# Kernel optimization log

Hardware: AMD Instinct MI355X
Metric: run time of the kernel (lower is better)

The kernel has to match this reference:

```python
import jax, jax.numpy as jnp
import numpy as np

N = 50000   # nodes
E = 800000  # edges
D = 128     # hidden_dim
LN_EPS = 1e-5


def _mlp2(x, W1, b1, W2, b2, act_last):
    y = jax.nn.silu(x @ W1 + b1)
    y = y @ W2 + b2
    return jax.nn.silu(y) if act_last else y


def setup_inputs() -> dict:
    key = jax.random.key(0)
    ks = jax.random.split(key, 20)
    s = 1.0 / np.sqrt(D)
    inp = {
        "h": jax.random.normal(ks[0], (N, D), jnp.float32),
        "x": jax.random.normal(ks[1], (N, 3), jnp.float32),
        "vel_all": jax.random.normal(ks[2], (N, 5, 3), jnp.float32),
        "edge_index": jax.random.randint(ks[3], (2, E), 0, N, jnp.int64),
        # phi_e: Linear(2D+11, D) -> SiLU -> Linear(D, D) -> SiLU   (weights stored [in,out])
        "We1": jax.random.uniform(ks[4], (2 * D + 11, D), jnp.float32, -s, s),
        "be1": jax.random.uniform(ks[5], (D,), jnp.float32, -s, s),
        "We2": jax.random.uniform(ks[6], (D, D), jnp.float32, -s, s),
        "be2": jax.random.uniform(ks[7], (D,), jnp.float32, -s, s),
        # phi_x: Linear(D, D) -> SiLU -> Linear(D, 1)
        "Wx1": jax.random.uniform(ks[8], (D, D), jnp.float32, -s, s),
        "bx1": jax.random.uniform(ks[9], (D,), jnp.float32, -s, s),
        "Wx2": jax.random.uniform(ks[10], (D, 1), jnp.float32, -s, s),
        "bx2": jax.random.uniform(ks[11], (1,), jnp.float32, -s, s),
        # phi_h: Linear(2D, D) -> SiLU -> Linear(D, D)
        "Wh1": jax.random.uniform(ks[12], (2 * D, D), jnp.float32, -s, s),
        "bh1": jax.random.uniform(ks[13], (D,), jnp.float32, -s, s),
        "Wh2": jax.random.uniform(ks[14], (D, D), jnp.float32, -s, s),
        "bh2": jax.random.uniform(ks[15], (D,), jnp.float32, -s, s),
        # LayerNorm(D)
        "gamma": jnp.ones((D,), jnp.float32),
        "beta": jnp.zeros((D,), jnp.float32),
    }
    return inp


def reference(h, x, vel_all, edge_index, We1, be1, We2, be2, Wx1, bx1, Wx2, bx2,
              Wh1, bh1, Wh2, bh2, gamma, beta):
    n = h.shape[0]
    src, dst = edge_index[0], edge_index[1]

    rel = x[src] - x[dst]                                  # [E,3]
    dist2 = jnp.sum(rel * rel, axis=-1, keepdims=True)     # [E,1]
    dist = jnp.maximum(jnp.sqrt(dist2), 1e-8)
    r_hat = rel / dist                                     # [E,3]

    vel_proj_src = jnp.sum(vel_all[src] * r_hat[:, None, :], axis=-1)  # [E,5]
    vel_proj_dst = jnp.sum(vel_all[dst] * r_hat[:, None, :], axis=-1)  # [E,5]

    feat = jnp.concatenate([h[src], h[dst], dist2, vel_proj_src, vel_proj_dst], axis=-1)
    m_ij = _mlp2(feat, We1, be1, We2, be2, act_last=True)  # [E,D]

    # update_coords=True: scatter_mean of rel * phi_x(m_ij)
    coord_w = _mlp2(m_ij, Wx1, bx1, Wx2, bx2, act_last=False)          # [E,1]
    num = jax.ops.segment_sum(rel * coord_w, dst, num_segments=n)      # [N,3]
    cnt = jax.ops.segment_sum(jnp.ones((rel.shape[0], 1), x.dtype), dst, num_segments=n)
    delta_x = num / jnp.maximum(cnt, 1.0)
    x = x + delta_x

    agg = jax.ops.segment_sum(m_ij, dst, num_segments=n)               # [N,D]
    dh = _mlp2(jnp.concatenate([h, agg], axis=-1), Wh1, bh1, Wh2, bh2, act_last=False)
    h = h + dh  # dropout=0 -> identity

    # LayerNorm
    mu = jnp.mean(h, axis=-1, keepdims=True)
    var = jnp.mean(jnp.square(h - mu), axis=-1, keepdims=True)
    h = (h - mu) * jax.lax.rsqrt(var + LN_EPS) * gamma + beta

    return (h, x, m_ij)
```

## Files before the change

### kernel.cpp

```cpp
#include <hip/hip_runtime.h>
#include <stdint.h>

#define CAPB 64

typedef __attribute__((ext_vector_type(8))) short bf16x8;
typedef __attribute__((ext_vector_type(4))) float f32x4;

__device__ __forceinline__ float bf2f(unsigned short u){
  union { unsigned int i; float f; } v; v.i = ((unsigned int)u) << 16; return v.f;
}
__device__ __forceinline__ unsigned short f2bf(float f){
  union { float f; unsigned int i; } v; v.f = f;
  unsigned int x = v.i;
  unsigned int r = (x + 0x7FFFu + ((x >> 16) & 1u)) >> 16;
  return (unsigned short)r;
}
__device__ __forceinline__ float silu_f(float v){
  return v / (1.0f + __expf(-v));
}

template<bool F32> __device__ __forceinline__ float ldv(const void* p, size_t i){
  if (F32) return ((const float*)p)[i];
  return bf2f(((const unsigned short*)p)[i]);
}
template<bool F32> __device__ __forceinline__ void stv(void* p, size_t i, float v){
  if (F32) ((float*)p)[i] = v;
  else     ((unsigned short*)p)[i] = f2bf(v);
}
template<bool I64> __device__ __forceinline__ int ldidx(const int* p, size_t i){
  return I64 ? p[2*i] : p[i];
}

__global__ void detect_kernel(const unsigned int* gw, const int* eidx, int N, int* flags){
  int f = 0;
  if (gw[0] == 0x3F800000u) f |= 1;
  bool i64 = true;
  for (int k = 0; k < 4; k++){
    int lo = eidx[2*k], hi = eidx[2*k+1];
    if (hi != 0 || lo < 0 || lo >= N) i64 = false;
  }
  if (i64) f |= 2;
  flags[0] = f;
}

__global__ __launch_bounds__(256) void hist_kernel(
    const int* eidx, int* cnt_i, int* bucket, int* slot, int N, int E, const int* flags)
{
  int e = blockIdx.x * 256 + threadIdx.x;
  if (e >= E) return;
  int d;
  if (flags[0] & 2) d = eidx[2*((size_t)E + e)];
  else              d = eidx[(size_t)E + e];
  d = min(max(d, 0), N-1);
  int p = atomicAdd(&cnt_i[d], 1);
  slot[e] = p;
  if (p < CAPB) bucket[(size_t)d*CAPB + p] = e;
}

struct __align__(16) NodePreSmem { float hlt[128][36]; };

template<bool F32>
__device__ void node_pre_impl(NodePreSmem& S, const void* h, const void* We1,
                              unsigned short* H1a, unsigned short* H1b, int N)
{
  const int t = threadIdx.x;
  const int base = blockIdx.x * 32;
  for (int i = t; i < 32*128; i += 256){
    int nl = i >> 7, j = i & 127;
    int node = base + nl;
    S.hlt[j][nl] = (node < N) ? ldv<F32>(h, (size_t)node*128 + j) : 0.0f;
  }
  __syncthreads();
  const int j = t & 127, half = t >> 7;
  const size_t wbase = (size_t)(half * 128) * 128;
  unsigned short* O = half ? H1b : H1a;
  float acc[32];
  #pragma unroll
  for (int nl=0; nl<32; nl++) acc[nl] = 0.0f;
  #pragma unroll 2
  for (int k=0; k<128; k++){
    float w = ldv<F32>(We1, wbase + (size_t)k*128 + j);
    const float4* row = (const float4*)&S.hlt[k][0];
    #pragma unroll
    for (int g=0; g<8; g++){
      float4 hv = row[g];
      acc[g*4+0] += hv.x * w;
      acc[g*4+1] += hv.y * w;
      acc[g*4+2] += hv.z * w;
      acc[g*4+3] += hv.w * w;
    }
  }
  #pragma unroll
  for (int nl=0; nl<32; nl++){
    int node = base + nl;
    if (node < N) O[(size_t)node*128 + j] = f2bf(acc[nl]);
  }
}

__global__ __launch_bounds__(256) void node_pre(
    const void* h, const void* We1, unsigned short* H1a, unsigned short* H1b,
    int N, const int* flags)
{
  __shared__ NodePreSmem S;
  if (flags[0] & 1) node_pre_impl<true >(S, h, We1, H1a, H1b, N);
  else              node_pre_impl<false>(S, h, We1, H1a, H1b, N);
}

template<bool F32, bool I64, bool M1F32>
__device__ void m1_impl(
    const void* xu, const void* velu, const int* eidx,
    const unsigned short* __restrict__ H1a, const unsigned short* __restrict__ H1b,
    const void* We1, const void* be1,
    void* m1p, int N, int E)
{
  const int t = threadIdx.x;
  const int sub = t & 31;
  const int j0 = sub * 4;
  float gw[11][4];
  #pragma unroll
  for (int k=0;k<11;k++)
    #pragma unroll
    for (int c=0;c<4;c++) gw[k][c] = ldv<F32>(We1, (size_t)(256+k)*128 + j0 + c);
  float b1[4];
  #pragma unroll
  for (int c=0;c<4;c++) b1[c] = ldv<F32>(be1, j0 + c);

  int gid = blockIdx.x * 8 + (t >> 5);
  const int gstride = gridDim.x * 8;
  for (int e = gid; e < E; e += gstride){
    int s = ldidx<I64>(eidx, e);
    int d = ldidx<I64>(eidx, (size_t)E + e);
    s = min(max(s, 0), N-1);
    d = min(max(d, 0), N-1);
    float rx = ldv<F32>(xu,(size_t)s*3+0) - ldv<F32>(xu,(size_t)d*3+0);
    float ry = ldv<F32>(xu,(size_t)s*3+1) - ldv<F32>(xu,(size_t)d*3+1);
    float rz = ldv<F32>(xu,(size_t)s*3+2) - ldv<F32>(xu,(size_t)d*3+2);
    float dist2 = rx*rx + ry*ry + rz*rz;
    float dist = fmaxf(sqrtf(dist2), 1e-8f);
    float inv = 1.0f / dist;
    float ux = rx*inv, uy = ry*inv, uz = rz*inv;
    float geo[11];
    geo[0] = dist2;
    #pragma unroll
    for (int v=0; v<5; v++){
      geo[1+v] = ldv<F32>(velu,(size_t)s*15+v*3+0)*ux + ldv<F32>(velu,(size_t)s*15+v*3+1)*uy + ldv<F32>(velu,(size_t)s*15+v*3+2)*uz;
      geo[6+v] = ldv<F32>(velu,(size_t)d*15+v*3+0)*ux + ldv<F32>(velu,(size_t)d*15+v*3+1)*uy + ldv<F32>(velu,(size_t)d*15+v*3+2)*uz;
    }
    uint2 ua = *(const uint2*)&H1a[(size_t)s*128 + j0];
    uint2 ub = *(const uint2*)&H1b[(size_t)d*128 + j0];
    float a[4];
    a[0] = bf2f((unsigned short)(ua.x & 0xFFFFu)) + bf2f((unsigned short)(ub.x & 0xFFFFu)) + b1[0];
    a[1] = bf2f((unsigned short)(ua.x >> 16))     + bf2f((unsigned short)(ub.x >> 16))     + b1[1];
    a[2] = bf2f((unsigned short)(ua.y & 0xFFFFu)) + bf2f((unsigned short)(ub.y & 0xFFFFu)) + b1[2];
    a[3] = bf2f((unsigned short)(ua.y >> 16))     + bf2f((unsigned short)(ub.y >> 16))     + b1[3];
    #pragma unroll
    for (int k=0;k<11;k++){
      float g = geo[k];
      #pragma unroll
      for (int c=0;c<4;c++) a[c] += gw[k][c] * g;
    }
    #pragma unroll
    for (int c=0;c<4;c++) a[c] = silu_f(a[c]);
    if (M1F32){
      float4 v = { a[0], a[1], a[2], a[3] };
      *(float4*)((float*)m1p + (size_t)e*128 + j0) = v;
    } else {
      uint2 p;
      p.x = (unsigned int)f2bf(a[0]) | ((unsigned int)f2bf(a[1]) << 16);
      p.y = (unsigned int)f2bf(a[2]) | ((unsigned int)f2bf(a[3]) << 16);
      *(uint2*)((unsigned short*)m1p + (size_t)e*128 + j0) = p;
    }
  }
}

template<bool USE_WS>
__global__ __launch_bounds__(256) void m1_kernel(
    const void* xu, const void* velu, const int* eidx,
    const unsigned short* H1a, const unsigned short* H1b,
    const void* We1, const void* be1,
    void* m1ws, void* out, size_t moff, int N, int E, const int* flags)
{
  int f = flags[0];
  if (USE_WS){
    if      (f == 0) m1_impl<false,false,false>(xu,velu,eidx,H1a,H1b,We1,be1,m1ws,N,E);
    else if (f == 1) m1_impl<true ,false,false>(xu,velu,eidx,H1a,H1b,We1,be1,m1ws,N,E);
    else if (f == 2) m1_impl<false,true ,false>(xu,velu,eidx,H1a,H1b,We1,be1,m1ws,N,E);
    else             m1_impl<true ,true ,false>(xu,velu,eidx,H1a,H1b,We1,be1,m1ws,N,E);
  } else {
    if (f & 1){
      void* p = (void*)((float*)out + moff);
      if (f & 2) m1_impl<true,true ,true>(xu,velu,eidx,H1a,H1b,We1,be1,p,N,E);
      else       m1_impl<true,false,true>(xu,velu,eidx,H1a,H1b,We1,be1,p,N,E);
    } else {
      void* p = (void*)((unsigned short*)out + moff);
      if (f & 2) m1_impl<false,true ,false>(xu,velu,eidx,H1a,H1b,We1,be1,p,N,E);
      else       m1_impl<false,false,false>(xu,velu,eidx,H1a,H1b,We1,be1,p,N,E);
    }
  }
}

struct __align__(16) GemmSmem {
  unsigned short m1s[64][136];
  unsigned short m2s[64][136];
  float relv[192];
  int   dsts[64];
  int   slot[64];
  float wpart[4][64];
};

template<bool F32, bool I64, bool M1F32>
__device__ void gemm_impl(GemmSmem& S,
    const void* xu, const int* eidx, const void* m1p,
    const void* We2, const void* be2, const void* Wx1, const void* bx1,
    const void* Wx2, const void* bx2,
    void* out, size_t moff,
    float* __restrict__ agg, float* __restrict__ num,
    const int* __restrict__ slotp,
    int N, int E, int ntiles)
{
  const int t = threadIdx.x;
  const int wave = t >> 6, lane = t & 63;
  const int col = lane & 15, quad = lane >> 4;
  const int colbase = wave * 32;

  bf16x8 bwe2[2][4], bwx1[2][4];
  float wx2v[2], be2v[2], bx1v[2];
  #pragma unroll
  for (int nt=0; nt<2; nt++){
    int n = colbase + nt*16 + col;
    wx2v[nt] = ldv<F32>(Wx2, n);
    be2v[nt] = ldv<F32>(be2, n);
    bx1v[nt] = ldv<F32>(bx1, n);
    #pragma unroll
    for (int kb=0; kb<4; kb++){
      bf16x8 a, b;
      #pragma unroll
      for (int jj=0; jj<8; jj++){
        int k = kb*32 + quad*8 + jj;
        a[jj] = (short)f2bf(ldv<F32>(We2, (size_t)k*128 + n));
        b[jj] = (short)f2bf(ldv<F32>(Wx1, (size_t)k*128 + n));
      }
      bwe2[nt][kb] = a; bwx1[nt][kb] = b;
    }
  }
  const int jfix = t & 127;
  const float bx2v = ldv<F32>(bx2, 0);
  const int srow = t >> 2, sseg = t & 3;

  for (int tile = blockIdx.x; tile < ntiles; tile += gridDim.x){
    const int ebase = tile * 64;
    {
      const int e = ebase + srow;
      if (M1F32){
        const float* rp = (const float*)m1p + (size_t)e*128 + sseg*32;
        #pragma unroll
        for (int q=0;q<4;q++){
          float4 va = {0,0,0,0}, vb = {0,0,0,0};
          if (e < E){ va = *(const float4*)(rp + q*8); vb = *(const float4*)(rp + q*8 + 4); }
          bf16x8 w;
          w[0]=(short)f2bf(va.x); w[1]=(short)f2bf(va.y); w[2]=(short)f2bf(va.z); w[3]=(short)f2bf(va.w);
          w[4]=(short)f2bf(vb.x); w[5]=(short)f2bf(vb.y); w[6]=(short)f2bf(vb.z); w[7]=(short)f2bf(vb.w);
          *(bf16x8*)&S.m1s[srow][sseg*32 + q*8] = w;
        }
      } else {
        const unsigned short* rp = (const unsigned short*)m1p + (size_t)e*128 + sseg*32;
        #pragma unroll
        for (int q=0;q<4;q++){
          bf16x8 w = {0,0,0,0,0,0,0,0};
          if (e < E) w = *(const bf16x8*)(rp + q*8);
          *(bf16x8*)&S.m1s[srow][sseg*32 + q*8] = w;
        }
      }
      if (t < 64){
        int e2 = ebase + t;
        int s2 = 0, d2 = 0, sl = 0;
        if (e2 < E){
          s2 = ldidx<I64>(eidx, e2);
          d2 = ldidx<I64>(eidx, (size_t)E + e2);
          sl = slotp[e2];
        }
        s2 = min(max(s2,0), N-1); d2 = min(max(d2,0), N-1);
        S.dsts[t] = d2; S.slot[t] = sl;
        S.relv[t*3+0] = ldv<F32>(xu,(size_t)s2*3+0) - ldv<F32>(xu,(size_t)d2*3+0);
        S.relv[t*3+1] = ldv<F32>(xu,(size_t)s2*3+1) - ldv<F32>(xu,(size_t)d2*3+1);
        S.relv[t*3+2] = ldv<F32>(xu,(size_t)s2*3+2) - ldv<F32>(xu,(size_t)d2*3+2);
      }
    }
    __syncthreads();
    #pragma unroll
    for (int et=0; et<4; et++){
      #pragma unroll
      for (int nt=0; nt<2; nt++){
        f32x4 acc = { be2v[nt], be2v[nt], be2v[nt], be2v[nt] };
        #pragma unroll
        for (int kb=0; kb<4; kb++){
          bf16x8 a = *(const bf16x8*)&S.m1s[et*16 + col][kb*32 + quad*8];
          acc = __builtin_amdgcn_mfma_f32_16x16x32_bf16(a, bwe2[nt][kb], acc, 0, 0, 0);
        }
        int n = colbase + nt*16 + col;
        #pragma unroll
        for (int r=0; r<4; r++)
          S.m2s[et*16 + quad*4 + r][n] = f2bf(silu_f(acc[r]));
      }
    }
    __syncthreads();
    if (F32){
      #pragma unroll
      for (int it=0; it<4; it++){
        const int sl = t + it*256;
        const int el = sl >> 4, i8 = sl & 15;
        const int e = ebase + el;
        if (e < E){
          const bf16x8 mv = *(const bf16x8*)&S.m2s[el][i8*8];
          float f[8];
          #pragma unroll
          for (int j=0; j<8; j++) f[j] = bf2f((unsigned short)mv[j]);
          float* op = (float*)out + moff + (size_t)e*128 + i8*8;
          float4 v0 = { f[0], f[1], f[2], f[3] };
          float4 v1 = { f[4], f[5], f[6], f[7] };
          *(float4*)op = v0;
          *(float4*)(op + 4) = v1;
          if (S.slot[el] >= CAPB){
            float* ap = &agg[(size_t)S.dsts[el]*128 + i8*8];
            #pragma unroll
            for (int j=0; j<8; j++) atomicAdd(ap + j, f[j]);
          }
        }
      }
    } else {
      #pragma unroll
      for (int it=0; it<32; it++){
        int el = (t + it*256) >> 7;
        int e = ebase + el;
        if (e < E){
          float v = bf2f(S.m2s[el][jfix]);
          stv<F32>(out, moff + (size_t)e*128 + jfix, v);
          atomicAdd(&agg[(size_t)S.dsts[el]*128 + jfix], v);
        }
      }
    }
    float part[4][4];
    #pragma unroll
    for (int et=0; et<4; et++)
      #pragma unroll
      for (int r=0; r<4; r++) part[et][r] = 0.0f;
    #pragma unroll
    for (int et=0; et<4; et++){
      #pragma unroll
      for (int nt=0; nt<2; nt++){
        f32x4 acc = { bx1v[nt], bx1v[nt], bx1v[nt], bx1v[nt] };
        #pragma unroll
        for (int kb=0; kb<4; kb++){
          bf16x8 a = *(const bf16x8*)&S.m2s[et*16 + col][kb*32 + quad*8];
          acc = __builtin_amdgcn_mfma_f32_16x16x32_bf16(a, bwx1[nt][kb], acc, 0, 0, 0);
        }
        #pragma unroll
        for (int r=0; r<4; r++) part[et][r] += silu_f(acc[r]) * wx2v[nt];
      }
    }
    #pragma unroll
    for (int et=0; et<4; et++){
      #pragma unroll
      for (int r=0; r<4; r++){
        float v = part[et][r];
        v += __shfl_xor(v, 1, 16);
        v += __shfl_xor(v, 2, 16);
        v += __shfl_xor(v, 4, 16);
        v += __shfl_xor(v, 8, 16);
        part[et][r] = v;
      }
    }
    if (col == 0){
      #pragma unroll
      for (int et=0; et<4; et++)
        #pragma unroll
        for (int r=0; r<4; r++)
          S.wpart[wave][et*16 + quad*4 + r] = part[et][r];
    }
    __syncthreads();
    if (t < 64){
      int e = ebase + t;
      if (e < E){
        float w = S.wpart[0][t] + S.wpart[1][t] + S.wpart[2][t] + S.wpart[3][t] + bx2v;
        int d = S.dsts[t];
        atomicAdd(&num[(size_t)d*3+0], S.relv[t*3+0]*w);
        atomicAdd(&num[(size_t)d*3+1], S.relv[t*3+1]*w);
        atomicAdd(&num[(size_t)d*3+2], S.relv[t*3+2]*w);
      }
    }
    __syncthreads();
  }
}

template<bool USE_WS>
__global__ __launch_bounds__(256) void gemm_kernel(
    const void* xu, const int* eidx, const void* m1ws,
    const void* We2, const void* be2, const void* Wx1, const void* bx1,
    const void* Wx2, const void* bx2,
    void* out, size_t moff, float* agg, float* num, const int* slotp,
    int N, int E, int ntiles, const int* flags)
{
  __shared__ GemmSmem S;
  int f = flags[0];
  if (USE_WS){
    if      (f == 0) gemm_impl<false,false,false>(S, xu, eidx, m1ws, We2,be2,Wx1,bx1,Wx2,bx2, out,moff, agg,num, slotp, N,E,ntiles);
    else if (f == 1) gemm_impl<true ,false,false>(S, xu, eidx, m1ws, We2,be2,Wx1,bx1,Wx2,bx2, out,moff, agg,num, slotp, N,E,ntiles);
    else if (f == 2) gemm_impl<false,true ,false>(S, xu, eidx, m1ws, We2,be2,Wx1,bx1,Wx2,bx2, out,moff, agg,num, slotp, N,E,ntiles);
    else             gemm_impl<true ,true ,false>(S, xu, eidx, m1ws, We2,be2,Wx1,bx1,Wx2,bx2, out,moff, agg,num, slotp, N,E,ntiles);
  } else {
    if (f & 1){
      const void* p = (const void*)((float*)out + moff);
      if (f & 2) gemm_impl<true,true ,true>(S, xu, eidx, p, We2,be2,Wx1,bx1,Wx2,bx2, out,moff, agg,num, slotp, N,E,ntiles);
      else       gemm_impl<true,false,true>(S, xu, eidx, p, We2,be2,Wx1,bx1,Wx2,bx2, out,moff, agg,num, slotp, N,E,ntiles);
    } else {
      const void* p = (const void*)((unsigned short*)out + moff);
      if (f & 2) gemm_impl<false,true ,false>(S, xu, eidx, p, We2,be2,Wx1,bx1,Wx2,bx2, out,moff, agg,num, slotp, N,E,ntiles);
      else       gemm_impl<false,false,false>(S, xu, eidx, p, We2,be2,Wx1,bx1,Wx2,bx2, out,moff, agg,num, slotp, N,E,ntiles);
    }
  }
}

struct __align__(16) NodeFinalSmem {
  unsigned short ins[16][256];
  unsigned short y1s[16][128];
  float hns[16][128];
};

template<bool F32>
__device__ void node_final_impl(NodeFinalSmem& S,
    const void* h, const void* xu,
    const float* __restrict__ agg, const float* __restrict__ num,
    const int* __restrict__ cnt_i, const int* __restrict__ bucket,
    const void* Wh1, const void* bh1, const void* Wh2, const void* bh2,
    const void* gam, const void* bet,
    void* out, size_t xoff, size_t moff, int N)
{
  const int t = threadIdx.x;
  const int base = blockIdx.x * 16;
  for (int i = t; i < 16*128; i += 256){
    int n = i >> 7, c = i & 127;
    int node = base + n;
    S.ins[n][c] = (node < N) ? f2bf(ldv<F32>(h, (size_t)node*128 + c)) : (unsigned short)0;
  }
  if (F32){
    const int g = t >> 4, i8 = t & 15;
    const int lanebase = (t & 63) & ~15;
    const int node = base + g;
    float a[8] = {0,0,0,0,0,0,0,0};
    if (node < N){
      int deg = cnt_i[node];
      int kmax = min(deg, CAPB);
      const float* mbase = (const float*)out + moff;
      for (int c0 = 0; c0 < kmax; c0 += 16){
        int ee = 0;
        if (c0 + i8 < kmax) ee = bucket[(size_t)node*CAPB + c0 + i8];
        int cnum = min(16, kmax - c0);
        #pragma unroll
        for (int k = 0; k < 16; k++){
          if (k < cnum){
            int e = __shfl(ee, lanebase + k, 64);
            const float* rp = mbase + (size_t)e*128 + i8*8;
            float4 v0 = *(const float4*)rp;
            float4 v1 = *(const float4*)(rp + 4);
            a[0]+=v0.x; a[1]+=v0.y; a[2]+=v0.z; a[3]+=v0.w;
            a[4]+=v1.x; a[5]+=v1.y; a[6]+=v1.z; a[7]+=v1.w;
          }
        }
      }
      if (deg > CAPB){
        const float* ap = &agg[(size_t)node*128 + i8*8];
        #pragma unroll
        for (int j=0; j<8; j++) a[j] += ap[j];
      }
    }
    #pragma unroll
    for (int j=0; j<8; j++) S.ins[g][128 + i8*8 + j] = f2bf(a[j]);
  } else {
    for (int i = t; i < 16*128; i += 256){
      int n = i >> 7, c = i & 127;
      int node = base + n;
      S.ins[n][128 + c] = (node < N) ? f2bf(agg[(size_t)node*128 + c]) : (unsigned short)0;
    }
  }
  __syncthreads();
  const int j = t & 127, nh = t >> 7;
  {
    float acc[8];
    #pragma unroll
    for (int u=0; u<8; u++) acc[u] = ldv<F32>(bh1, j);
    #pragma unroll 4
    for (int k=0; k<256; k++){
      float w = ldv<F32>(Wh1, (size_t)k*128 + j);
      #pragma unroll
      for (int u=0; u<8; u++) acc[u] += bf2f(S.ins[nh + 2*u][k]) * w;
    }
    #pragma unroll
    for (int u=0; u<8; u++) S.y1s[nh + 2*u][j] = f2bf(silu_f(acc[u]));
  }
  __syncthreads();
  {
    float acc[8];
    #pragma unroll
    for (int u=0; u<8; u++) acc[u] = ldv<F32>(bh2, j);
    #pragma unroll 4
    for (int k=0; k<128; k++){
      float w = ldv<F32>(Wh2, (size_t)k*128 + j);
      #pragma unroll
      for (int u=0; u<8; u++) acc[u] += bf2f(S.y1s[nh + 2*u][k]) * w;
    }
    #pragma unroll
    for (int u=0; u<8; u++){
      int n = nh + 2*u;
      int node = base + n;
      float hv = (node < N) ? ldv<F32>(h, (size_t)node*128 + j) : 0.0f;
      S.hns[n][j] = hv + acc[u];
    }
  }
  __syncthreads();
  {
    int n = t >> 4, sub = t & 15;
    float s = 0.0f, ss = 0.0f;
    #pragma unroll
    for (int i2=0; i2<8; i2++){
      float v = S.hns[n][sub + 16*i2];
      s += v; ss += v*v;
    }
    #pragma unroll
    for (int m=1; m<16; m<<=1){ s += __shfl_xor(s, m, 16); ss += __shfl_xor(ss, m, 16); }
    float mu = s * (1.0f/128.0f);
    float var = fmaxf(ss * (1.0f/128.0f) - mu*mu, 0.0f);
    float rs = rsqrtf(var + 1e-5f);
    int gnode = base + n;
    if (gnode < N){
      #pragma unroll
      for (int i2=0; i2<8; i2++){
        int jj = sub + 16*i2;
        float v = (S.hns[n][jj] - mu) * rs * ldv<F32>(gam, jj) + ldv<F32>(bet, jj);
        stv<F32>(out, (size_t)gnode*128 + jj, v);
      }
    }
  }
  if (t < 48){
    int n = t / 3, c = t % 3;
    int node = base + n;
    if (node < N){
      float cv = fmaxf((float)cnt_i[node], 1.0f);
      float dx = num[(size_t)node*3 + c] / cv;
      stv<F32>(out, xoff + (size_t)node*3 + c, ldv<F32>(xu, (size_t)node*3 + c) + dx);
    }
  }
}

__global__ __launch_bounds__(256) void node_final(
    const void* h, const void* xu,
    const float* agg, const float* num, const int* cnt_i, const int* bucket,
    const void* Wh1, const void* bh1, const void* Wh2, const void* bh2,
    const void* gam, const void* bet,
    void* out, size_t xoff, size_t moff, int N, const int* flags)
{
  __shared__ NodeFinalSmem S;
  if (flags[0] & 1) node_final_impl<true >(S, h, xu, agg, num, cnt_i, bucket, Wh1, bh1, Wh2, bh2, gam, bet, out, xoff, moff, N);
  else              node_final_impl<false>(S, h, xu, agg, num, cnt_i, bucket, Wh1, bh1, Wh2, bh2, gam, bet, out, xoff, moff, N);
}

extern "C" void kernel_launch(void* const* d_in, const int* in_sizes, int n_in,
                              void* d_out, int out_size, void* d_ws, size_t ws_size,
                              hipStream_t stream)
{
  const int N = in_sizes[0] / 128;
  const int E = in_sizes[3] / 2;

  char* ws = (char*)d_ws;
  int* flags = (int*)ws;
  size_t off = 256;
  unsigned short* H1a = (unsigned short*)(ws + off); off += (size_t)N*256;
  unsigned short* H1b = (unsigned short*)(ws + off); off += (size_t)N*256;
  float* agg   = (float*)(ws + off); off += (size_t)N*512;
  float* num   = (float*)(ws + off); off += (size_t)N*12;
  int*   cnt_i = (int*)(ws + off); off += (size_t)N*4;
  int*   bucket= (int*)(ws + off); off += (size_t)N*CAPB*4;
  int*   slot  = (int*)(ws + off); off += (size_t)E*4;
  void*  m1ws  = (void*)(ws + off); off += (size_t)E*256;
  const bool use_ws = (off <= ws_size);

  detect_kernel<<<1, 1, 0, stream>>>((const unsigned int*)d_in[16], (const int*)d_in[3], N, flags);

  size_t zbytes = (size_t)N*512 + (size_t)N*12 + (size_t)N*4;
  hipMemsetAsync((void*)agg, 0, zbytes, stream);

  hist_kernel<<<(E + 255) / 256, 256, 0, stream>>>((const int*)d_in[3], cnt_i, bucket, slot, N, E, flags);

  node_pre<<<(N + 31) / 32, 256, 0, stream>>>(d_in[0], d_in[4], H1a, H1b, N, flags);

  size_t xoff = (size_t)N * 128;
  size_t moff = (size_t)N * 128 + (size_t)N * 3;
  int ntiles = (E + 63) / 64;

  if (use_ws){
    m1_kernel<true><<<2048, 256, 0, stream>>>(d_in[1], d_in[2], (const int*)d_in[3], H1a, H1b,
                                              d_in[4], d_in[5], m1ws, d_out, moff, N, E, flags);
    gemm_kernel<true><<<2500, 256, 0, stream>>>(d_in[1], (const int*)d_in[3], m1ws,
                                                d_in[6], d_in[7], d_in[8], d_in[9],
                                                d_in[10], d_in[11],
                                                d_out, moff, agg, num, slot, N, E, ntiles, flags);
  } else {
    m1_kernel<false><<<2048, 256, 0, stream>>>(d_in[1], d_in[2], (const int*)d_in[3], H1a, H1b,
                                               d_in[4], d_in[5], m1ws, d_out, moff, N, E, flags);
    gemm_kernel<false><<<2500, 256, 0, stream>>>(d_in[1], (const int*)d_in[3], m1ws,
                                                 d_in[6], d_in[7], d_in[8], d_in[9],
                                                 d_in[10], d_in[11],
                                                 d_out, moff, agg, num, slot, N, E, ntiles, flags);
  }

  node_final<<<(N + 15) / 16, 256, 0, stream>>>(d_in[0], d_in[1], agg, num, cnt_i, bucket,
                                                d_in[12], d_in[13], d_in[14], d_in[15],
                                                d_in[16], d_in[17],
                                                d_out, xoff, moff, N, flags);
}
```

Measured before the change: 1.311 ms.

## Software-pipeline m1 tile loads and defer coord atomics in edge GEMM kernel

Adds a specialized fp32-input path for the edge GEMM kernel. It prefetches the next tile's bf16 m1 rows and edge indices into registers while the current tile runs its MFMA work. The num coordinate atomics are deferred by one iteration so they overlap the next tile's setup instead of needing an extra barrier. This costs more registers per thread, which may lower occupancy, and makes the loop carry state across iterations.

```diff
diff --git a/kernel.cpp b/kernel.cpp
--- a/kernel.cpp
+++ b/kernel.cpp
@@ -207,6 +207,172 @@
   int   slot[64];
   float wpart[4][64];
 };
+
+template<bool I64>
+__device__ void gemm_async_impl(GemmSmem& S,
+    const float* __restrict__ xu, const int* __restrict__ eidx,
+    const unsigned short* __restrict__ m1p,
+    const float* __restrict__ We2, const float* __restrict__ be2,
+    const float* __restrict__ Wx1, const float* __restrict__ bx1,
+    const float* __restrict__ Wx2, const float* __restrict__ bx2,
+    float* __restrict__ out, size_t moff,
+    float* __restrict__ agg, float* __restrict__ num,
+    const int* __restrict__ slotp,
+    int N, int E, int ntiles)
+{
+  const int t = threadIdx.x;
+  const int wave = t >> 6, lane = t & 63;
+  const int col = lane & 15, quad = lane >> 4;
+  const int colbase = wave * 32;
+
+  bf16x8 bwe2[2][4], bwx1[2][4];
+  float wx2v[2], be2v[2], bx1v[2];
+  #pragma unroll
+  for (int nt=0; nt<2; nt++){
+    int n = colbase + nt*16 + col;
+    wx2v[nt] = Wx2[n]; be2v[nt] = be2[n]; bx1v[nt] = bx1[n];
+    #pragma unroll
+    for (int kb=0; kb<4; kb++){
+      bf16x8 a, b;
+      #pragma unroll
+      for (int jj=0; jj<8; jj++){
+        int k = kb*32 + quad*8 + jj;
+        a[jj] = (short)f2bf(We2[(size_t)k*128 + n]);
+        b[jj] = (short)f2bf(Wx1[(size_t)k*128 + n]);
+      }
+      bwe2[nt][kb] = a; bwx1[nt][kb] = b;
+    }
+  }
+  const float bx2v = bx2[0];
+  const int srow = t >> 2, sseg = t & 3;
+  const int gs = gridDim.x;
+
+  bf16x8 r0, r1, r2, r3;
+  int nsv = 0, ndv = 0, nsl = 0;
+  float prx = 0, pry = 0, prz = 0;
+  int pdst = 0, pvalid = 0, have_w = 0;
+
+  int tile = blockIdx.x;
+  if (tile < ntiles){
+    size_t e = (size_t)tile*64 + srow; if (e >= (size_t)E) e = (size_t)E - 1;
+    const unsigned short* rp = m1p + e*128 + (size_t)sseg*32;
+    r0 = *(const bf16x8*)(rp);      r1 = *(const bf16x8*)(rp + 8);
+    r2 = *(const bf16x8*)(rp + 16); r3 = *(const bf16x8*)(rp + 24);
+    if (t < 64){
+      int ec = min(tile*64 + t, E-1);
+      nsv = ldidx<I64>(eidx, ec);
+      ndv = ldidx<I64>(eidx, (size_t)E + ec);
+      nsl = slotp[ec];
+    }
+  }
+
+  for (; tile < ntiles; tile += gs){
+    const int ebase = tile * 64;
+    if (t < 64){
+      if (have_w && pvalid){
+        float w = S.wpart[0][t] + S.wpart[1][t] + S.wpart[2][t] + S.wpart[3][t] + bx2v;
+        atomicAdd(&num[(size_t)pdst*3+0], prx*w);
+        atomicAdd(&num[(size_t)pdst*3+1], pry*w);
+        atomicAdd(&num[(size_t)pdst*3+2], prz*w);
+      }
+      int s = min(max(nsv, 0), N-1), d = min(max(ndv, 0), N-1);
+      S.dsts[t] = d; S.slot[t] = nsl;
+      pvalid = (ebase + t) < E; pdst = d;
+      prx = xu[(size_t)s*3+0] - xu[(size_t)d*3+0];
+      pry = xu[(size_t)s*3+1] - xu[(size_t)d*3+1];
+      prz = xu[(size_t)s*3+2] - xu[(size_t)d*3+2];
+    }
+    *(bf16x8*)&S.m1s[srow][sseg*32 +  0] = r0;
+    *(bf16x8*)&S.m1s[srow][sseg*32 +  8] = r1;
+    *(bf16x8*)&S.m1s[srow][sseg*32 + 16] = r2;
+    *(bf16x8*)&S.m1s[srow][sseg*32 + 24] = r3;
+    if (tile + gs < ntiles){
+      size_t e = (size_t)(tile+gs)*64 + srow; if (e >= (size_t)E) e = (size_t)E - 1;
+      const unsigned short* rp = m1p + e*128 + (size_t)sseg*32;
+      r0 = *(const bf16x8*)(rp);      r1 = *(const bf16x8*)(rp + 8);
+      r2 = *(const bf16x8*)(rp + 16); r3 = *(const bf16x8*)(rp + 24);
+      if (t < 64){
+        int ec = min((tile+gs)*64 + t, E-1);
+        nsv = ldidx<I64>(eidx, ec);
+        ndv = ldidx<I64>(eidx, (size_t)E + ec);
+        nsl = slotp[ec];
+      }
+    }
+    __syncthreads();
+    const int erem = E - ebase;
+    #pragma unroll
+    for (int et=0; et<4; et++){
+      #pragma unroll
+      for (int nt=0; nt<2; nt++){
+        f32x4 acc = { be2v[nt], be2v[nt], be2v[nt], be2v[nt] };
+        #pragma unroll
+        for (int kb=0; kb<4; kb++){
+          bf16x8 a = *(const bf16x8*)&S.m1s[et*16 + col][kb*32 + quad*8];
+          acc = __builtin_amdgcn_mfma_f32_16x16x32_bf16(a, bwe2[nt][kb], acc, 0, 0, 0);
+        }
+        int n = colbase + nt*16 + col;
+        #pragma unroll
+        for (int r=0; r<4; r++){
+          int el = et*16 + quad*4 + r;
+          float v = silu_f(acc[r]);
+          S.m2s[el][n] = f2bf(v);
+          if (el < erem){
+            out[moff + (size_t)(ebase + el)*128 + n] = v;
+            if (S.slot[el] >= CAPB)
+              atomicAdd(&agg[(size_t)S.dsts[el]*128 + n], v);
+          }
+        }
+      }
+    }
+    __syncthreads();
+    float part[4][4];
+    #pragma unroll
+    for (int et=0; et<4; et++)
+      #pragma unroll
+      for (int r=0; r<4; r++) part[et][r] = 0.0f;
+    #pragma unroll
+    for (int et=0; et<4; et++){
+      #pragma unroll
+      for (int nt=0; nt<2; nt++){
+        f32x4 acc = { bx1v[nt], bx1v[nt], bx1v[nt], bx1v[nt] };
+        #pragma unroll
+        for (int kb=0; kb<4; kb++){
+          bf16x8 a = *(const bf16x8*)&S.m2s[et*16 + col][kb*32 + quad*8];
+          acc = __builtin_amdgcn_mfma_f32_16x16x32_bf16(a, bwx1[nt][kb], acc, 0, 0, 0);
+        }
+        #pragma unroll
+        for (int r=0; r<4; r++) part[et][r] += silu_f(acc[r]) * wx2v[nt];
+      }
+    }
+    #pragma unroll
+    for (int et=0; et<4; et++){
+      #pragma unroll
+      for (int r=0; r<4; r++){
+        float v = part[et][r];
+        v += __shfl_xor(v, 1, 16);
+        v += __shfl_xor(v, 2, 16);
+        v += __shfl_xor(v, 4, 16);
+        v += __shfl_xor(v, 8, 16);
+        part[et][r] = v;
+      }
+    }
+    if (col == 0){
+      #pragma unroll
+      for (int et=0; et<4; et++)
+        #pragma unroll
+        for (int r=0; r<4; r++)
+          S.wpart[wave][et*16 + quad*4 + r] = part[et][r];
+    }
+    __syncthreads();
+    have_w = 1;
+  }
+  if (t < 64 && have_w && pvalid){
+    float w = S.wpart[0][t] + S.wpart[1][t] + S.wpart[2][t] + S.wpart[3][t] + bx2v;
+    atomicAdd(&num[(size_t)pdst*3+0], prx*w);
+    atomicAdd(&num[(size_t)pdst*3+1], pry*w);
+    atomicAdd(&num[(size_t)pdst*3+2], prz*w);
+  }
+}
 
 template<bool F32, bool I64, bool M1F32>
 __device__ void gemm_impl(GemmSmem& S,
@@ -402,11 +568,18 @@
 {
   __shared__ GemmSmem S;
   int f = flags[0];
-  if (USE_WS){
-    if      (f == 0) gemm_impl<false,false,false>(S, xu, eidx, m1ws, We2,be2,Wx1,bx1,Wx2,bx2, out,moff, agg,num, slotp, N,E,ntiles);
-    else if (f == 1) gemm_impl<true ,false,false>(S, xu, eidx, m1ws, We2,be2,Wx1,bx1,Wx2,bx2, out,moff, agg,num, slotp, N,E,ntiles);
-    else if (f == 2) gemm_impl<false,true ,false>(S, xu, eidx, m1ws, We2,be2,Wx1,bx1,Wx2,bx2, out,moff, agg,num, slotp, N,E,ntiles);
-    else             gemm_impl<true ,true ,false>(S, xu, eidx, m1ws, We2,be2,Wx1,bx1,Wx2,bx2, out,moff, agg,num, slotp, N,E,ntiles);
+  if (USE_WS && (f & 1)){
+    if (f & 2) gemm_async_impl<true >(S, (const float*)xu, eidx, (const unsigned short*)m1ws,
+                                      (const float*)We2,(const float*)be2,(const float*)Wx1,(const float*)bx1,
+                                      (const float*)Wx2,(const float*)bx2,
+                                      (float*)out, moff, agg, num, slotp, N, E, ntiles);
+    else       gemm_async_impl<false>(S, (const float*)xu, eidx, (const unsigned short*)m1ws,
+                                      (const float*)We2,(const float*)be2,(const float*)Wx1,(const float*)bx1,
+                                      (const float*)Wx2,(const float*)bx2,
+                                      (float*)out, moff, agg, num, slotp, N, E, ntiles);
+  } else if (USE_WS){
+    if (f & 2) gemm_impl<false,true ,false>(S, xu, eidx, m1ws, We2,be2,Wx1,bx1,Wx2,bx2, out,moff, agg,num, slotp, N,E,ntiles);
+    else       gemm_impl<false,false,false>(S, xu, eidx, m1ws, We2,be2,Wx1,bx1,Wx2,bx2, out,moff, agg,num, slotp, N,E,ntiles);
   } else {
     if (f & 1){
       const void* p = (const void*)((float*)out + moff);
```

Result: slower. 1.356 ms (+3.5%).
